# Kernel tuning notes

Measured on AMD Instinct MI355X. Metric: run time of the kernel, lower is better.

The kernel has to match this reference:

```python
import jax, jax.numpy as jnp
import numpy as np

N = 1_000_000
VOCAB = 50_000
EMBED_DIM = 128
ENCODE_DIM = 128


def _random_preorder_tree(n, seed=0):
    """Generate a random tree whose nodes are numbered in pre-order DFS.
    Returns subtree_end[i] = index of the last node in node i's subtree (inclusive)."""
    rng = np.random.default_rng(seed)
    parent = np.empty(n, dtype=np.int64)
    parent[0] = -1
    stack = [0]
    pops = rng.geometric(0.5, size=n) - 1  # how far up to climb before attaching
    for i in range(1, n):
        npop = min(int(pops[i]), len(stack) - 1)
        for _ in range(npop):
            stack.pop()
        parent[i] = stack[-1]
        stack.append(i)
    end = np.arange(n, dtype=np.int64)
    for i in range(n - 1, 0, -1):
        p = parent[i]
        if end[p] < end[i]:
            end[p] = end[i]
    return end


def setup_inputs() -> dict:
    key = jax.random.key(0)
    k1, k2, k3, k4 = jax.random.split(key, 4)
    tokens = jax.random.randint(k1, (N,), 0, VOCAB, dtype=jnp.int64).astype(jnp.int32)
    subtree_end = jnp.asarray(_random_preorder_tree(N), dtype=jnp.int32)
    embedding_weight = jax.random.normal(k2, (VOCAB, EMBED_DIM), dtype=jnp.float32)
    W = jax.random.normal(k3, (ENCODE_DIM, EMBED_DIM), dtype=jnp.float32) * (1.0 / np.sqrt(EMBED_DIM))
    b = jax.random.normal(k4, (ENCODE_DIM,), dtype=jnp.float32) * 0.01
    return {"tokens": tokens, "subtree_end": subtree_end,
            "embedding_weight": embedding_weight, "W": W, "b": b}


def reference(tokens, subtree_end, embedding_weight, W, b):
    # Per-node contribution: x_i = Linear(Embed(token_i))          [N, encode_dim]
    x = embedding_weight[tokens] @ W.T + b
    # h_i = sum of x over subtree(i). With pre-order DFS numbering, the subtree
    # of i is the contiguous range [i, subtree_end[i]], so use an inclusive
    # prefix sum: h_i = S[end_i] - S[i] + x_i.
    S = jnp.cumsum(x, axis=0)                                      # [N, encode_dim]
    h = S[subtree_end] - S + x                                     # [N, encode_dim]
    # pool = max over all node hidden states (order-independent)
    return jnp.max(h, axis=0)                                      # [encode_dim]
```

## Files before the change

### kernel.cpp

```cpp
#include <hip/hip_runtime.h>
#include <hip/hip_bf16.h>

#define D      128
#define LG     9
#define CHUNK  512

typedef __attribute__((ext_vector_type(8))) short          short8;
typedef __attribute__((ext_vector_type(8))) unsigned short ushort8;
typedef __attribute__((ext_vector_type(4))) float          floatx4;

__device__ inline float b2f(unsigned short u) {
    return __uint_as_float(((unsigned)u) << 16);
}
__device__ inline short f2bf(float f) {
    __hip_bfloat16 h = __float2bfloat16(f);
    unsigned short u;
    __builtin_memcpy(&u, &h, 2);
    return (short)u;
}

__global__ void init_out_kernel(float* out, int out_size) {
    int t = threadIdx.x;
    if (t < out_size) out[t] = -INFINITY;
}

__global__ void local_scan_kernel(const int* __restrict__ tokens,
                                  const float* __restrict__ emb,
                                  unsigned short* __restrict__ S,
                                  float* __restrict__ sumE, int n) {
    __shared__ int toks[CHUNK];
    int c  = blockIdx.x;
    int i0 = c << LG;
    int cnt = min(CHUNK, n - i0);
    for (int t = threadIdx.x; t < cnt; t += 128) toks[t] = tokens[i0 + t];
    __syncthreads();
    int d = threadIdx.x;
    float run = 0.f;
    #pragma unroll 8
    for (int j = 0; j < cnt; ++j) {
        run += emb[(size_t)toks[j] * D + d];
        S[(size_t)(i0 + j) * D + d] = (unsigned short)f2bf(run);
    }
    sumE[(size_t)c * D + d] = run;
}

__global__ void scan_kernel(float* sumE, int C) {
    int d    = blockIdx.x;
    int lane = threadIdx.x;
    float carry = 0.f;
    for (int c0 = 0; c0 < C; c0 += 64) {
        int c = c0 + lane;
        float v = (c < C) ? sumE[(size_t)c * D + d] : 0.f;
        float incl = v;
        #pragma unroll
        for (int off = 1; off < 64; off <<= 1) {
            float t = __shfl_up(incl, off);
            if (lane >= off) incl += t;
        }
        if (c < C) sumE[(size_t)c * D + d] = carry + incl - v;
        carry += __shfl(incl, 63);
    }
}

__device__ inline void atomicMaxF(float* addr, float v) {
    if (v >= 0.f) atomicMax((int*)addr, __float_as_int(v));
    else          atomicMin((unsigned int*)addr, __float_as_uint(v));
}

__global__ __launch_bounds__(256, 2) void max_pass_kernel(
        const int* __restrict__ ends, const unsigned short* __restrict__ S,
        const float* __restrict__ prefE, const float* __restrict__ W,
        const float* __restrict__ bvec, float* __restrict__ out,
        int n, int n_tiles, int tpp) {
    __shared__ float red[4][4][16];
    int tid  = threadIdx.x;
    int lane = tid & 63;
    int wid  = tid >> 6;
    int c  = lane & 15;
    int kg = lane >> 4;
    int tw   = wid & 1;
    int pair = blockIdx.x * 2 + (wid >> 1);

    short8 Wf[4][4];
    float  bc[4];
    #pragma unroll
    for (int tl = 0; tl < 4; ++tl) {
        int tg = tw * 4 + tl;
        const float* wr = W + (size_t)(tg * 16 + c) * D + kg * 8;
        bc[tl] = bvec[tg * 16 + c];
        #pragma unroll
        for (int kk = 0; kk < 4; ++kk) {
            floatx4 f0 = *(const floatx4*)(wr + kk * 32);
            floatx4 f1 = *(const floatx4*)(wr + kk * 32 + 4);
            short8 w;
            #pragma unroll
            for (int j = 0; j < 4; ++j) { w[j] = f2bf(f0[j]); w[j + 4] = f2bf(f1[j]); }
            Wf[tl][kk] = w;
        }
    }
    float mx[4];
    #pragma unroll
    for (int tl = 0; tl < 4; ++tl) mx[tl] = -INFINITY;

    int t0 = pair * tpp;
    int t1 = min(n_tiles, t0 + tpp);
    if (t0 < t1) {
        int e_cur = ends[min(t0 * 16 + c, n - 1)];
        for (int tt = t0; tt < t1; ++tt) {
            int base = tt * 16;
            int node = base + c;
            bool vr  = node < n;
            int e = e_cur;
            int nidx = (tt + 1 < t1) ? (tt + 1) * 16 + c : node;
            int e_next = ends[min(nidx, n - 1)];
            int p  = node - 1;
            int pc = max(p, 0);
            int ce = e >> LG, cp = pc >> LG;
            bool fast = __all(vr && p >= 0 && ce == cp);
            const ushort8* pe = (const ushort8*)(S + (size_t)e  * D) + kg;
            const ushort8* pp = (const ushort8*)(S + (size_t)pc * D) + kg;
            short8 A[4];
            if (fast) {
                #pragma unroll
                for (int kk = 0; kk < 4; ++kk) {
                    ushort8 se = pe[kk * 4];
                    ushort8 sp = pp[kk * 4];
                    short8 a;
                    #pragma unroll
                    for (int j = 0; j < 8; ++j)
                        a[j] = f2bf(b2f(se[j]) - b2f(sp[j]));
                    A[kk] = a;
                }
            } else {
                const float* qe = prefE + (size_t)ce * D + kg * 8;
                const float* qp = prefE + (size_t)cp * D + kg * 8;
                float vmask = vr ? 1.f : 0.f;
                float pmask = (p >= 0) ? 1.f : 0.f;
                #pragma unroll
                for (int kk = 0; kk < 4; ++kk) {
                    ushort8 se = pe[kk * 4];
                    ushort8 sp = pp[kk * 4];
                    floatx4 qe0 = *(const floatx4*)(qe + kk * 32);
                    floatx4 qe1 = *(const floatx4*)(qe + kk * 32 + 4);
                    floatx4 qp0 = *(const floatx4*)(qp + kk * 32);
                    floatx4 qp1 = *(const floatx4*)(qp + kk * 32 + 4);
                    short8 a;
                    #pragma unroll
                    for (int j = 0; j < 4; ++j) {
                        float fe0 = b2f(se[j])     + qe0[j];
                        float fp0 = b2f(sp[j])     + qp0[j];
                        float fe1 = b2f(se[j + 4]) + qe1[j];
                        float fp1 = b2f(sp[j + 4]) + qp1[j];
                        a[j]     = f2bf(vmask * (fe0 - pmask * fp0));
                        a[j + 4] = f2bf(vmask * (fe1 - pmask * fp1));
                    }
                    A[kk] = a;
                }
            }
            floatx4 cnt;
            #pragma unroll
            for (int i = 0; i < 4; ++i) {
                int nd = base + kg * 4 + i;
                float ee = (float)__shfl(e, kg * 4 + i);
                cnt[i] = (nd < n) ? (ee - (float)nd + 1.f) : 0.f;
            }
            #pragma unroll
            for (int tl = 0; tl < 4; ++tl) {
                floatx4 acc = {0.f, 0.f, 0.f, 0.f};
                acc = __builtin_amdgcn_mfma_f32_16x16x32_bf16(A[0], Wf[tl][0], acc, 0, 0, 0);
                acc = __builtin_amdgcn_mfma_f32_16x16x32_bf16(A[1], Wf[tl][1], acc, 0, 0, 0);
                acc = __builtin_amdgcn_mfma_f32_16x16x32_bf16(A[2], Wf[tl][2], acc, 0, 0, 0);
                acc = __builtin_amdgcn_mfma_f32_16x16x32_bf16(A[3], Wf[tl][3], acc, 0, 0, 0);
                #pragma unroll
                for (int i = 0; i < 4; ++i) {
                    int nd = base + kg * 4 + i;
                    float h = acc[i] + cnt[i] * bc[tl];
                    if (nd < n) mx[tl] = fmaxf(mx[tl], h);
                }
            }
            e_cur = e_next;
        }
    }
    #pragma unroll
    for (int tl = 0; tl < 4; ++tl) {
        float v = mx[tl];
        v = fmaxf(v, __shfl_xor(v, 16));
        v = fmaxf(v, __shfl_xor(v, 32));
        mx[tl] = v;
    }
    if (kg == 0) {
        #pragma unroll
        for (int tl = 0; tl < 4; ++tl) red[wid][tl][c] = mx[tl];
    }
    __syncthreads();
    if (tid < 128) {
        int twf = tid >> 6;
        int tl  = (tid >> 4) & 3;
        int cc  = tid & 15;
        float v = fmaxf(red[twf][tl][cc], red[twf + 2][tl][cc]);
        atomicMaxF(&out[(twf * 4 + tl) * 16 + cc], v);
    }
}

extern "C" void kernel_launch(void* const* d_in, const int* in_sizes, int n_in,
                              void* d_out, int out_size, void* d_ws, size_t ws_size,
                              hipStream_t stream) {
    const int*   tokens = (const int*)d_in[0];
    const int*   ends   = (const int*)d_in[1];
    const float* emb    = (const float*)d_in[2];
    const float* W      = (const float*)d_in[3];
    const float* bvec   = (const float*)d_in[4];
    float* out = (float*)d_out;
    int n = in_sizes[0];
    int C = (n + CHUNK - 1) >> LG;

    unsigned short* S    = (unsigned short*)d_ws;
    float*          sumE = (float*)(S + (size_t)n * D);

    init_out_kernel<<<1, 128, 0, stream>>>(out, out_size);
    local_scan_kernel<<<C, 128, 0, stream>>>(tokens, emb, S, sumE, n);
    scan_kernel<<<128, 64, 0, stream>>>(sumE, C);

    int n_tiles = (n + 15) / 16;
    int nblocks = 512;
    int pairs   = nblocks * 2;
    int tpp = (n_tiles + pairs - 1) / pairs;
    max_pass_kernel<<<nblocks, 256, 0, stream>>>(ends, S, sumE, W, bvec, out,
                                                 n, n_tiles, tpp);
}
```

Measured before the change: 310.8 us.

## Stage chunk prefix rows in swizzled LDS and compute max pass per chunk

The max pass now runs one block per 256-node chunk instead of a fixed grid of 512 blocks. Each block stages that chunk's bf16 local prefix rows and end indices into XOR-swizzled shared memory, so S[end] and S[i-1] are read from LDS instead of as scattered global gathers. Ends that fall outside the chunk use a global gather plus chunk offsets. The subtraction moves after the matmul by running two MFMA chains (end and prev rows), which doubles matrix work but drops the per-element bf16 difference. The chunk size also halves, giving more blocks for the local scan but more chunk boundaries.

```diff
diff --git a/kernel.cpp b/kernel.cpp
--- a/kernel.cpp
+++ b/kernel.cpp
@@ -2,8 +2,8 @@
 #include <hip/hip_bf16.h>
 
 #define D      128
-#define LG     9
-#define CHUNK  512
+#define LG     8
+#define CHUNK  256
 
 typedef __attribute__((ext_vector_type(8))) short          short8;
 typedef __attribute__((ext_vector_type(8))) unsigned short ushort8;
@@ -70,16 +70,34 @@
 __global__ __launch_bounds__(256, 2) void max_pass_kernel(
         const int* __restrict__ ends, const unsigned short* __restrict__ S,
         const float* __restrict__ prefE, const float* __restrict__ W,
-        const float* __restrict__ bvec, float* __restrict__ out,
-        int n, int n_tiles, int tpp) {
+        const float* __restrict__ bvec, float* __restrict__ out, int n) {
+    __shared__ ushort8 Sl[257 * 16];
+    __shared__ int   s_end[CHUNK];
     __shared__ float red[4][4][16];
-    int tid  = threadIdx.x;
-    int lane = tid & 63;
-    int wid  = tid >> 6;
+    int tid = threadIdx.x;
+    int cb  = blockIdx.x;
+    int i0  = cb << LG;
+    int cnt = min(CHUNK, n - i0);
+
+    for (int t = tid; t < CHUNK; t += 256)
+        s_end[t] = (i0 + t < n) ? ends[i0 + t] : (i0 + t);
+    const ushort8* gsrc = (const ushort8*)(S + (size_t)i0 * D);
+    int units = cnt * 16;
+    for (int u = tid; u < units; u += 256) {
+        int r = u >> 4, q = u & 15;
+        Sl[(r << 4) | (q ^ (r & 7))] = gsrc[u];
+    }
+    ushort8 z = {0, 0, 0, 0, 0, 0, 0, 0};
+    for (int u = units + tid; u < 257 * 16; u += 256) {
+        int r = u >> 4, q = u & 15;
+        Sl[(r << 4) | (q ^ (r & 7))] = z;
+    }
+
+    int lane = tid & 63, wid = tid >> 6;
     int c  = lane & 15;
     int kg = lane >> 4;
     int tw   = wid & 1;
-    int pair = blockIdx.x * 2 + (wid >> 1);
+    int pair = wid >> 1;
 
     short8 Wf[4][4];
     float  bc[4];
@@ -102,83 +120,74 @@
     #pragma unroll
     for (int tl = 0; tl < 4; ++tl) mx[tl] = -INFINITY;
 
-    int t0 = pair * tpp;
-    int t1 = min(n_tiles, t0 + tpp);
-    if (t0 < t1) {
-        int e_cur = ends[min(t0 * 16 + c, n - 1)];
-        for (int tt = t0; tt < t1; ++tt) {
-            int base = tt * 16;
-            int node = base + c;
-            bool vr  = node < n;
-            int e = e_cur;
-            int nidx = (tt + 1 < t1) ? (tt + 1) * 16 + c : node;
-            int e_next = ends[min(nidx, n - 1)];
-            int p  = node - 1;
-            int pc = max(p, 0);
-            int ce = e >> LG, cp = pc >> LG;
-            bool fast = __all(vr && p >= 0 && ce == cp);
-            const ushort8* pe = (const ushort8*)(S + (size_t)e  * D) + kg;
-            const ushort8* pp = (const ushort8*)(S + (size_t)pc * D) + kg;
-            short8 A[4];
-            if (fast) {
+    __syncthreads();
+
+    int tiles = (cnt + 15) >> 4;
+    int Tend  = min(pair * 8 + 8, tiles);
+    for (int T = pair * 8; T < Tend; ++T) {
+        int j    = (T << 4) + c;
+        int node = i0 + j;
+        bool vr  = node < n;
+        int e    = s_end[j];
+        int eloc = e - i0;
+        bool cross = vr && (eloc >= CHUNK);
+        int re = cross ? j : eloc;
+        int rp = (j == 0) ? 256 : (j - 1);
+
+        short8 Ae[4], Ap[4];
+        #pragma unroll
+        for (int kk = 0; kk < 4; ++kk) {
+            ushort8 ve = Sl[(re << 4) | ((kk * 4 + kg) ^ (re & 7))];
+            ushort8 vp = Sl[(rp << 4) | ((kk * 4 + kg) ^ (rp & 7))];
+            __builtin_memcpy(&Ae[kk], &ve, 16);
+            __builtin_memcpy(&Ap[kk], &vp, 16);
+        }
+        if (cross) {
+            int ce = e >> LG;
+            const ushort8* ge = (const ushort8*)(S + (size_t)e * D);
+            const float* qe = prefE + (size_t)ce * D + kg * 8;
+            const float* qc = prefE + (size_t)cb * D + kg * 8;
+            #pragma unroll
+            for (int kk = 0; kk < 4; ++kk) {
+                ushort8 se = ge[kk * 4 + kg];
+                floatx4 qe0 = *(const floatx4*)(qe + kk * 32);
+                floatx4 qe1 = *(const floatx4*)(qe + kk * 32 + 4);
+                floatx4 qc0 = *(const floatx4*)(qc + kk * 32);
+                floatx4 qc1 = *(const floatx4*)(qc + kk * 32 + 4);
+                short8 a;
                 #pragma unroll
-                for (int kk = 0; kk < 4; ++kk) {
-                    ushort8 se = pe[kk * 4];
-                    ushort8 sp = pp[kk * 4];
-                    short8 a;
-                    #pragma unroll
-                    for (int j = 0; j < 8; ++j)
-                        a[j] = f2bf(b2f(se[j]) - b2f(sp[j]));
-                    A[kk] = a;
+                for (int jj = 0; jj < 4; ++jj) {
+                    a[jj]     = f2bf(b2f(se[jj])     + qe0[jj] - qc0[jj]);
+                    a[jj + 4] = f2bf(b2f(se[jj + 4]) + qe1[jj] - qc1[jj]);
                 }
-            } else {
-                const float* qe = prefE + (size_t)ce * D + kg * 8;
-                const float* qp = prefE + (size_t)cp * D + kg * 8;
-                float vmask = vr ? 1.f : 0.f;
-                float pmask = (p >= 0) ? 1.f : 0.f;
-                #pragma unroll
-                for (int kk = 0; kk < 4; ++kk) {
-                    ushort8 se = pe[kk * 4];
-                    ushort8 sp = pp[kk * 4];
-                    floatx4 qe0 = *(const floatx4*)(qe + kk * 32);
-                    floatx4 qe1 = *(const floatx4*)(qe + kk * 32 + 4);
-                    floatx4 qp0 = *(const floatx4*)(qp + kk * 32);
-                    floatx4 qp1 = *(const floatx4*)(qp + kk * 32 + 4);
-                    short8 a;
-                    #pragma unroll
-                    for (int j = 0; j < 4; ++j) {
-                        float fe0 = b2f(se[j])     + qe0[j];
-                        float fp0 = b2f(sp[j])     + qp0[j];
-                        float fe1 = b2f(se[j + 4]) + qe1[j];
-                        float fp1 = b2f(sp[j + 4]) + qp1[j];
-                        a[j]     = f2bf(vmask * (fe0 - pmask * fp0));
-                        a[j + 4] = f2bf(vmask * (fe1 - pmask * fp1));
-                    }
-                    A[kk] = a;
-                }
+                Ae[kk] = a;
             }
-            floatx4 cnt;
+        }
+        floatx4 cnt4;
+        #pragma unroll
+        for (int i = 0; i < 4; ++i) {
+            int nd = i0 + (T << 4) + kg * 4 + i;
+            float ee = (float)__shfl(e, kg * 4 + i);
+            cnt4[i] = (nd < n) ? (ee - (float)nd + 1.f) : 0.f;
+        }
+        #pragma unroll
+        for (int tl = 0; tl < 4; ++tl) {
+            floatx4 ae = {0.f, 0.f, 0.f, 0.f};
+            floatx4 ap = {0.f, 0.f, 0.f, 0.f};
+            ae = __builtin_amdgcn_mfma_f32_16x16x32_bf16(Ae[0], Wf[tl][0], ae, 0, 0, 0);
+            ae = __builtin_amdgcn_mfma_f32_16x16x32_bf16(Ae[1], Wf[tl][1], ae, 0, 0, 0);
+            ae = __builtin_amdgcn_mfma_f32_16x16x32_bf16(Ae[2], Wf[tl][2], ae, 0, 0, 0);
+            ae = __builtin_amdgcn_mfma_f32_16x16x32_bf16(Ae[3], Wf[tl][3], ae, 0, 0, 0);
+            ap = __builtin_amdgcn_mfma_f32_16x16x32_bf16(Ap[0], Wf[tl][0], ap, 0, 0, 0);
+            ap = __builtin_amdgcn_mfma_f32_16x16x32_bf16(Ap[1], Wf[tl][1], ap, 0, 0, 0);
+            ap = __builtin_amdgcn_mfma_f32_16x16x32_bf16(Ap[2], Wf[tl][2], ap, 0, 0, 0);
+            ap = __builtin_amdgcn_mfma_f32_16x16x32_bf16(Ap[3], Wf[tl][3], ap, 0, 0, 0);
             #pragma unroll
             for (int i = 0; i < 4; ++i) {
-                int nd = base + kg * 4 + i;
-                float ee = (float)__shfl(e, kg * 4 + i);
-                cnt[i] = (nd < n) ? (ee - (float)nd + 1.f) : 0.f;
+                int nd = i0 + (T << 4) + kg * 4 + i;
+                float h = (ae[i] - ap[i]) + cnt4[i] * bc[tl];
+                if (nd < n) mx[tl] = fmaxf(mx[tl], h);
             }
-            #pragma unroll
-            for (int tl = 0; tl < 4; ++tl) {
-                floatx4 acc = {0.f, 0.f, 0.f, 0.f};
-                acc = __builtin_amdgcn_mfma_f32_16x16x32_bf16(A[0], Wf[tl][0], acc, 0, 0, 0);
-                acc = __builtin_amdgcn_mfma_f32_16x16x32_bf16(A[1], Wf[tl][1], acc, 0, 0, 0);
-                acc = __builtin_amdgcn_mfma_f32_16x16x32_bf16(A[2], Wf[tl][2], acc, 0, 0, 0);
-                acc = __builtin_amdgcn_mfma_f32_16x16x32_bf16(A[3], Wf[tl][3], acc, 0, 0, 0);
-                #pragma unroll
-                for (int i = 0; i < 4; ++i) {
-                    int nd = base + kg * 4 + i;
-                    float h = acc[i] + cnt[i] * bc[tl];
-                    if (nd < n) mx[tl] = fmaxf(mx[tl], h);
-                }
-            }
-            e_cur = e_next;
         }
     }
     #pragma unroll
@@ -220,11 +229,5 @@
     init_out_kernel<<<1, 128, 0, stream>>>(out, out_size);
     local_scan_kernel<<<C, 128, 0, stream>>>(tokens, emb, S, sumE, n);
     scan_kernel<<<128, 64, 0, stream>>>(sumE, C);
-
-    int n_tiles = (n + 15) / 16;
-    int nblocks = 512;
-    int pairs   = nblocks * 2;
-    int tpp = (n_tiles + pairs - 1) / pairs;
-    max_pass_kernel<<<nblocks, 256, 0, stream>>>(ends, S, sumE, W, bvec, out,
-                                                 n, n_tiles, tpp);
-}
+    max_pass_kernel<<<C, 256, 0, stream>>>(ends, S, sumE, W, bvec, out, n);
+}
```

After: 331.1 us. 1.07x slower.

## Double-buffer prefix-row loads, split MFMA by linearity, widen local scan

Applied to the files above, without the earlier changes.

The max pass now prefetches the next tile's two prefix-sum rows into a second register buffer while the current tile is computed. In the fast path it runs the MFMA on the end-row and predecessor-row bf16 values separately and subtracts the fp32 results, which removes the per-element subtract and bf16 re-rounding. The local scan gives each wave its own chunk (two chunks per 128-thread block), reads embeddings as float2 and writes packed bf16 pairs as 32-bit stores. The launch goes to 768 blocks with an occupancy hint of 3 and an even tiles-per-pair count. The cost is more registers for the double buffers, twice the MFMA count in the fast path, and redundant clamped loads past the final tile.

```diff
diff --git a/kernel.cpp b/kernel.cpp
--- a/kernel.cpp
+++ b/kernel.cpp
@@ -8,15 +8,23 @@
 typedef __attribute__((ext_vector_type(8))) short          short8;
 typedef __attribute__((ext_vector_type(8))) unsigned short ushort8;
 typedef __attribute__((ext_vector_type(4))) float          floatx4;
+typedef __attribute__((ext_vector_type(2))) float          floatx2;
 
 __device__ inline float b2f(unsigned short u) {
     return __uint_as_float(((unsigned)u) << 16);
 }
-__device__ inline short f2bf(float f) {
+__device__ inline unsigned short f2bf(float f) {
     __hip_bfloat16 h = __float2bfloat16(f);
     unsigned short u;
     __builtin_memcpy(&u, &h, 2);
-    return (short)u;
+    return u;
+}
+__device__ inline short8 u2s(ushort8 u) {
+    short8 s; __builtin_memcpy(&s, &u, 16); return s;
+}
+__device__ inline void atomicMaxF(float* addr, float v) {
+    if (v >= 0.f) atomicMax((int*)addr, __float_as_int(v));
+    else          atomicMin((unsigned int*)addr, __float_as_uint(v));
 }
 
 __global__ void init_out_kernel(float* out, int out_size) {
@@ -24,24 +32,25 @@
     if (t < out_size) out[t] = -INFINITY;
 }
 
-__global__ void local_scan_kernel(const int* __restrict__ tokens,
-                                  const float* __restrict__ emb,
-                                  unsigned short* __restrict__ S,
-                                  float* __restrict__ sumE, int n) {
-    __shared__ int toks[CHUNK];
-    int c  = blockIdx.x;
-    int i0 = c << LG;
-    int cnt = min(CHUNK, n - i0);
-    for (int t = threadIdx.x; t < cnt; t += 128) toks[t] = tokens[i0 + t];
-    __syncthreads();
-    int d = threadIdx.x;
-    float run = 0.f;
-    #pragma unroll 8
+__global__ __launch_bounds__(128) void local_scan_kernel(
+        const int* __restrict__ tokens, const float* __restrict__ emb,
+        unsigned* __restrict__ T32, float* __restrict__ sumE, int n, int C) {
+    __shared__ int toks[2][CHUNK];
+    int tid = threadIdx.x, w = tid >> 6, lane = tid & 63;
+    int cb = min(blockIdx.x * 2 + w, C - 1);
+    int i0 = cb << LG, cnt = min(CHUNK, n - i0);
+    for (int t = lane; t < cnt; t += 64) toks[w][t] = tokens[i0 + t];
+    const floatx2* eb = (const floatx2*)emb;
+    unsigned* To = T32 + (size_t)i0 * 64 + lane;
+    float rx = 0.f, ry = 0.f;
+    #pragma unroll 4
     for (int j = 0; j < cnt; ++j) {
-        run += emb[(size_t)toks[j] * D + d];
-        S[(size_t)(i0 + j) * D + d] = (unsigned short)f2bf(run);
-    }
-    sumE[(size_t)c * D + d] = run;
+        floatx2 v = eb[(size_t)toks[w][j] * 64 + lane];
+        rx += v[0]; ry += v[1];
+        To[(size_t)j * 64] = ((unsigned)f2bf(rx)) | (((unsigned)f2bf(ry)) << 16);
+    }
+    floatx2 rr = {rx, ry};
+    *(floatx2*)(sumE + (size_t)cb * D + lane * 2) = rr;
 }
 
 __global__ void scan_kernel(float* sumE, int C) {
@@ -62,39 +71,30 @@
     }
 }
 
-__device__ inline void atomicMaxF(float* addr, float v) {
-    if (v >= 0.f) atomicMax((int*)addr, __float_as_int(v));
-    else          atomicMin((unsigned int*)addr, __float_as_uint(v));
-}
-
-__global__ __launch_bounds__(256, 2) void max_pass_kernel(
+__global__ __launch_bounds__(256, 3) void max_pass_kernel(
         const int* __restrict__ ends, const unsigned short* __restrict__ S,
         const float* __restrict__ prefE, const float* __restrict__ W,
         const float* __restrict__ bvec, float* __restrict__ out,
-        int n, int n_tiles, int tpp) {
+        int n, int tpp) {
     __shared__ float red[4][4][16];
-    int tid  = threadIdx.x;
-    int lane = tid & 63;
-    int wid  = tid >> 6;
+    int tid = threadIdx.x, lane = tid & 63, wid = tid >> 6;
     int c  = lane & 15;
     int kg = lane >> 4;
-    int tw   = wid & 1;
-    int pair = blockIdx.x * 2 + (wid >> 1);
+    int tw = wid & 1, pair = wid >> 1;
 
     short8 Wf[4][4];
     float  bc[4];
     #pragma unroll
     for (int tl = 0; tl < 4; ++tl) {
-        int tg = tw * 4 + tl;
-        const float* wr = W + (size_t)(tg * 16 + c) * D + kg * 8;
-        bc[tl] = bvec[tg * 16 + c];
+        const float* wr = W + (size_t)((tw * 4 + tl) * 16 + c) * D + kg * 8;
+        bc[tl] = bvec[(tw * 4 + tl) * 16 + c];
         #pragma unroll
         for (int kk = 0; kk < 4; ++kk) {
             floatx4 f0 = *(const floatx4*)(wr + kk * 32);
             floatx4 f1 = *(const floatx4*)(wr + kk * 32 + 4);
             short8 w;
             #pragma unroll
-            for (int j = 0; j < 4; ++j) { w[j] = f2bf(f0[j]); w[j + 4] = f2bf(f1[j]); }
+            for (int j = 0; j < 4; ++j) { w[j] = (short)f2bf(f0[j]); w[j + 4] = (short)f2bf(f1[j]); }
             Wf[tl][kk] = w;
         }
     }
@@ -102,85 +102,100 @@
     #pragma unroll
     for (int tl = 0; tl < 4; ++tl) mx[tl] = -INFINITY;
 
-    int t0 = pair * tpp;
-    int t1 = min(n_tiles, t0 + tpp);
-    if (t0 < t1) {
-        int e_cur = ends[min(t0 * 16 + c, n - 1)];
-        for (int tt = t0; tt < t1; ++tt) {
-            int base = tt * 16;
-            int node = base + c;
-            bool vr  = node < n;
-            int e = e_cur;
-            int nidx = (tt + 1 < t1) ? (tt + 1) * 16 + c : node;
-            int e_next = ends[min(nidx, n - 1)];
-            int p  = node - 1;
-            int pc = max(p, 0);
-            int ce = e >> LG, cp = pc >> LG;
-            bool fast = __all(vr && p >= 0 && ce == cp);
-            const ushort8* pe = (const ushort8*)(S + (size_t)e  * D) + kg;
-            const ushort8* pp = (const ushort8*)(S + (size_t)pc * D) + kg;
-            short8 A[4];
-            if (fast) {
-                #pragma unroll
-                for (int kk = 0; kk < 4; ++kk) {
-                    ushort8 se = pe[kk * 4];
-                    ushort8 sp = pp[kk * 4];
-                    short8 a;
-                    #pragma unroll
-                    for (int j = 0; j < 8; ++j)
-                        a[j] = f2bf(b2f(se[j]) - b2f(sp[j]));
-                    A[kk] = a;
-                }
-            } else {
-                const float* qe = prefE + (size_t)ce * D + kg * 8;
-                const float* qp = prefE + (size_t)cp * D + kg * 8;
-                float vmask = vr ? 1.f : 0.f;
-                float pmask = (p >= 0) ? 1.f : 0.f;
-                #pragma unroll
-                for (int kk = 0; kk < 4; ++kk) {
-                    ushort8 se = pe[kk * 4];
-                    ushort8 sp = pp[kk * 4];
-                    floatx4 qe0 = *(const floatx4*)(qe + kk * 32);
-                    floatx4 qe1 = *(const floatx4*)(qe + kk * 32 + 4);
-                    floatx4 qp0 = *(const floatx4*)(qp + kk * 32);
-                    floatx4 qp1 = *(const floatx4*)(qp + kk * 32 + 4);
-                    short8 a;
-                    #pragma unroll
-                    for (int j = 0; j < 4; ++j) {
-                        float fe0 = b2f(se[j])     + qe0[j];
-                        float fp0 = b2f(sp[j])     + qp0[j];
-                        float fe1 = b2f(se[j + 4]) + qe1[j];
-                        float fp1 = b2f(sp[j + 4]) + qp1[j];
-                        a[j]     = f2bf(vmask * (fe0 - pmask * fp0));
-                        a[j + 4] = f2bf(vmask * (fe1 - pmask * fp1));
-                    }
-                    A[kk] = a;
-                }
-            }
-            floatx4 cnt;
-            #pragma unroll
-            for (int i = 0; i < 4; ++i) {
-                int nd = base + kg * 4 + i;
-                float ee = (float)__shfl(e, kg * 4 + i);
-                cnt[i] = (nd < n) ? (ee - (float)nd + 1.f) : 0.f;
-            }
-            #pragma unroll
-            for (int tl = 0; tl < 4; ++tl) {
-                floatx4 acc = {0.f, 0.f, 0.f, 0.f};
-                acc = __builtin_amdgcn_mfma_f32_16x16x32_bf16(A[0], Wf[tl][0], acc, 0, 0, 0);
-                acc = __builtin_amdgcn_mfma_f32_16x16x32_bf16(A[1], Wf[tl][1], acc, 0, 0, 0);
-                acc = __builtin_amdgcn_mfma_f32_16x16x32_bf16(A[2], Wf[tl][2], acc, 0, 0, 0);
-                acc = __builtin_amdgcn_mfma_f32_16x16x32_bf16(A[3], Wf[tl][3], acc, 0, 0, 0);
-                #pragma unroll
-                for (int i = 0; i < 4; ++i) {
-                    int nd = base + kg * 4 + i;
-                    float h = acc[i] + cnt[i] * bc[tl];
-                    if (nd < n) mx[tl] = fmaxf(mx[tl], h);
-                }
-            }
-            e_cur = e_next;
-        }
-    }
+    const ushort8* Sv = (const ushort8*)S;
+
+#define LD_E(tt) ends[min((tt) * 16 + c, n - 1)]
+#define LOAD_ROWS(tt, e, Pe, Pp) do {                                  \
+        int node_ = (tt) * 16 + c;                                     \
+        int pc_ = max(min(node_, n) - 1, 0);                           \
+        const ushort8* pe_ = Sv + (size_t)(e) * 16 + kg;               \
+        const ushort8* pp_ = Sv + (size_t)pc_ * 16 + kg;               \
+        Pe[0] = pe_[0]; Pe[1] = pe_[4]; Pe[2] = pe_[8]; Pe[3] = pe_[12]; \
+        Pp[0] = pp_[0]; Pp[1] = pp_[4]; Pp[2] = pp_[8]; Pp[3] = pp_[12]; \
+    } while (0)
+
+#define PROCESS(tt, e, Pe, Pp) do {                                    \
+        int base_ = (tt) * 16;                                         \
+        int node_ = base_ + c;                                         \
+        bool vr_  = node_ < n;                                         \
+        int p_  = node_ - 1;                                           \
+        int pc_ = max(p_, 0);                                          \
+        int ce_ = (e) >> LG, cp_ = pc_ >> LG;                          \
+        bool fast_ = __all(vr_ && p_ >= 0 && ce_ == cp_);              \
+        floatx4 cnt4_;                                                 \
+        _Pragma("unroll")                                              \
+        for (int i = 0; i < 4; ++i)                                    \
+            cnt4_[i] = (float)(__shfl((e), kg * 4 + i) - (base_ + kg * 4 + i) + 1); \
+        if (fast_) {                                                   \
+            _Pragma("unroll")                                          \
+            for (int tl = 0; tl < 4; ++tl) {                           \
+                floatx4 ae_ = {0.f, 0.f, 0.f, 0.f};                    \
+                floatx4 ap_ = {0.f, 0.f, 0.f, 0.f};                    \
+                _Pragma("unroll")                                      \
+                for (int kk = 0; kk < 4; ++kk) {                       \
+                    ae_ = __builtin_amdgcn_mfma_f32_16x16x32_bf16(u2s(Pe[kk]), Wf[tl][kk], ae_, 0, 0, 0); \
+                    ap_ = __builtin_amdgcn_mfma_f32_16x16x32_bf16(u2s(Pp[kk]), Wf[tl][kk], ap_, 0, 0, 0); \
+                }                                                      \
+                _Pragma("unroll")                                      \
+                for (int i = 0; i < 4; ++i) {                          \
+                    float h_ = (ae_[i] - ap_[i]) + cnt4_[i] * bc[tl];  \
+                    if (base_ + kg * 4 + i < n) mx[tl] = fmaxf(mx[tl], h_); \
+                }                                                      \
+            }                                                          \
+        } else {                                                       \
+            const float* qe_ = prefE + (size_t)ce_ * D + kg * 8;       \
+            const float* qp_ = prefE + (size_t)cp_ * D + kg * 8;       \
+            float vm_ = vr_ ? 1.f : 0.f;                               \
+            float pm_ = (p_ >= 0) ? 1.f : 0.f;                         \
+            short8 A_[4];                                              \
+            _Pragma("unroll")                                          \
+            for (int kk = 0; kk < 4; ++kk) {                           \
+                floatx4 qe0 = *(const floatx4*)(qe_ + kk * 32);        \
+                floatx4 qe1 = *(const floatx4*)(qe_ + kk * 32 + 4);    \
+                floatx4 qp0 = *(const floatx4*)(qp_ + kk * 32);        \
+                floatx4 qp1 = *(const floatx4*)(qp_ + kk * 32 + 4);    \
+                short8 a_;                                             \
+                _Pragma("unroll")                                      \
+                for (int j = 0; j < 4; ++j) {                          \
+                    float fe0 = b2f(Pe[kk][j])     + qe0[j];           \
+                    float fp0 = b2f(Pp[kk][j])     + qp0[j];           \
+                    float fe1 = b2f(Pe[kk][j + 4]) + qe1[j];           \
+                    float fp1 = b2f(Pp[kk][j + 4]) + qp1[j];           \
+                    a_[j]     = (short)f2bf(vm_ * (fe0 - pm_ * fp0));  \
+                    a_[j + 4] = (short)f2bf(vm_ * (fe1 - pm_ * fp1));  \
+                }                                                      \
+                A_[kk] = a_;                                           \
+            }                                                          \
+            _Pragma("unroll")                                          \
+            for (int tl = 0; tl < 4; ++tl) {                           \
+                floatx4 acc_ = {0.f, 0.f, 0.f, 0.f};                   \
+                _Pragma("unroll")                                      \
+                for (int kk = 0; kk < 4; ++kk)                         \
+                    acc_ = __builtin_amdgcn_mfma_f32_16x16x32_bf16(A_[kk], Wf[tl][kk], acc_, 0, 0, 0); \
+                _Pragma("unroll")                                      \
+                for (int i = 0; i < 4; ++i) {                          \
+                    float h_ = acc_[i] + cnt4_[i] * bc[tl];            \
+                    if (base_ + kg * 4 + i < n) mx[tl] = fmaxf(mx[tl], h_); \
+                }                                                      \
+            }                                                          \
+        }                                                              \
+    } while (0)
+
+    int t0 = (blockIdx.x * 2 + pair) * tpp;
+    ushort8 Ae[4], Ap[4], Be[4], Bp[4];
+    int e0 = LD_E(t0);
+    LOAD_ROWS(t0, e0, Ae, Ap);
+    int e1 = LD_E(t0 + 1);
+    for (int tt = t0; tt < t0 + tpp; tt += 2) {
+        LOAD_ROWS(tt + 1, e1, Be, Bp);
+        int e2 = LD_E(tt + 2);
+        PROCESS(tt, e0, Ae, Ap);
+        LOAD_ROWS(tt + 2, e2, Ae, Ap);
+        int e3 = LD_E(tt + 3);
+        PROCESS(tt + 1, e1, Be, Bp);
+        e0 = e2; e1 = e3;
+    }
+
     #pragma unroll
     for (int tl = 0; tl < 4; ++tl) {
         float v = mx[tl];
@@ -218,13 +233,14 @@
     float*          sumE = (float*)(S + (size_t)n * D);
 
     init_out_kernel<<<1, 128, 0, stream>>>(out, out_size);
-    local_scan_kernel<<<C, 128, 0, stream>>>(tokens, emb, S, sumE, n);
+    local_scan_kernel<<<(C + 1) / 2, 128, 0, stream>>>(tokens, emb,
+                                                       (unsigned*)S, sumE, n, C);
     scan_kernel<<<128, 64, 0, stream>>>(sumE, C);
 
     int n_tiles = (n + 15) / 16;
-    int nblocks = 512;
+    int nblocks = 768;
     int pairs   = nblocks * 2;
-    int tpp = (n_tiles + pairs - 1) / pairs;
+    int tpp = ((n_tiles + pairs - 1) / pairs + 1) & ~1;
     max_pass_kernel<<<nblocks, 256, 0, stream>>>(ends, S, sumE, W, bvec, out,
-                                                 n, n_tiles, tpp);
-}
+                                                 n, tpp);
+}
```

Result: slower. 401.6 us (+29.2%).
